# Kernel optimization log

Measured on AMD Instinct MI355X. Metric: run time of the kernel, lower is better.

Reference implementation:

```python
import jax, jax.numpy as jnp
import numpy as np

N_NODES = 50000      # also number of hyperedges (square incidence)
N_HEDGES = 50000
N_INC = 800000       # number of (node, hyperedge) incidences
N_LINKS = 20000
IN_DIM = 128         # edge_x dim; x dim is 2*IN_DIM
LATENT = [64, 64, 64]
HIDDEN = 256


def _hconv(x, src, dst, n_src, n_dst, W, b):
    """PyG HypergraphConv (no attention, unit hyperedge weights):
    out = D^{-1} H B^{-1} H^T (x W) + b, with src=node idx, dst=hyperedge idx."""
    xw = x @ W  # [n_src, out]
    ones = jnp.ones(src.shape[0], xw.dtype)
    Bdeg = jax.ops.segment_sum(ones, dst, num_segments=n_dst)
    Binv = jnp.where(Bdeg > 0, 1.0 / Bdeg, 0.0)
    Ddeg = jax.ops.segment_sum(ones, src, num_segments=n_src)
    Dinv = jnp.where(Ddeg > 0, 1.0 / Ddeg, 0.0)
    # node -> hyperedge aggregate, normalized by B^{-1}
    he = jax.ops.segment_sum(xw[src], dst, num_segments=n_dst) * Binv[:, None]
    # hyperedge -> node aggregate, normalized by D^{-1}
    out = jax.ops.segment_sum(he[dst], src, num_segments=n_src) * Dinv[:, None]
    return out + b


def setup_inputs() -> dict:
    key = jax.random.key(0)
    ks = jax.random.split(key, 24)
    inp = {
        "x": jax.random.normal(ks[0], (N_NODES, 2 * IN_DIM), jnp.float32),
        "edge_x": jax.random.normal(ks[1], (N_HEDGES, IN_DIM), jnp.float32),
        "edge_index": jax.random.randint(ks[2], (2, N_INC), 0, N_NODES, dtype=jnp.int32),
        "marks": jax.random.randint(ks[3], (N_LINKS,), 0, N_NODES, dtype=jnp.int32),
        "edge_marks": jax.random.randint(ks[4], (N_LINKS,), 0, N_HEDGES - 1, dtype=jnp.int32),
    }
    def lin(k, fin, fout):
        s = 1.0 / np.sqrt(fin)
        return jax.random.uniform(k, (fin, fout), jnp.float32, -s, s)
    # node convs: (2*IN_DIM -> 2*L0), (2*L0 -> 2*L1), (2*L1 -> 2*L2)
    nd = [2 * IN_DIM] + [2 * l for l in LATENT]
    ed = [IN_DIM] + list(LATENT)
    for i in range(3):
        inp[f"Wn{i}"] = lin(ks[5 + i], nd[i], nd[i + 1])
        inp[f"bn{i}"] = jnp.zeros((nd[i + 1],), jnp.float32)
        inp[f"We{i}"] = lin(ks[8 + i], ed[i], ed[i + 1])
        inp[f"be{i}"] = jnp.zeros((ed[i + 1],), jnp.float32)
    feat = sum(LATENT) * 4
    inp["W1"] = lin(ks[11], feat, HIDDEN)
    inp["b1"] = jnp.zeros((HIDDEN,), jnp.float32)
    inp["W2"] = lin(ks[12], HIDDEN, 2)
    inp["b2"] = jnp.zeros((2,), jnp.float32)
    return inp


def reference(x, edge_x, edge_index, marks, edge_marks,
              Wn0, bn0, Wn1, bn1, Wn2, bn2,
              We0, be0, We1, be1, We2, be2,
              W1, b1, W2, b2):
    nsrc, hdst = edge_index[0], edge_index[1]
    node_layers = [(Wn0, bn0), (Wn1, bn1), (Wn2, bn2)]
    edge_layers = [(We0, be0), (We1, be1), (We2, be2)]
    h, all_x = x, []
    for W, b in node_layers:
        h = jax.nn.relu(_hconv(h, nsrc, hdst, N_NODES, N_HEDGES, W, b))
        all_x.append(h)
    g, all_e = edge_x, []
    for W, b in edge_layers:  # flipped incidence: hyperedges act as nodes
        g = jax.nn.relu(_hconv(g, hdst, nsrc, N_HEDGES, N_NODES, W, b))
        all_e.append(g)
    xc = jnp.concatenate(all_x, axis=1)[marks]           # [L, 2*sum(latent)]
    ec = jnp.concatenate(all_e, axis=1)                  # [M, sum(latent)]
    a, b2_ = ec[edge_marks], ec[edge_marks + 1]
    feat = jnp.concatenate([jnp.minimum(a, b2_), jnp.maximum(a, b2_), xc], axis=1)
    h1 = jax.nn.relu(feat @ W1 + b1)
    logits = h1 @ W2 + b2
    return jax.nn.log_softmax(logits, axis=1)
```

## Files before the change

kernel.cpp:

```cpp
#include <hip/hip_runtime.h>
#include <hip/hip_fp16.h>
#include <math.h>

#define NN 50000
#define NH 50000
#define NI 800000
#define NL 20000

using half8 = __attribute__((ext_vector_type(8))) _Float16;
using f32x4 = __attribute__((ext_vector_type(4))) float;

static __device__ __forceinline__ float2 pack_h4(float4 v) {
    float2 st;
    *(__half2*)&st.x = __float22half2_rn(make_float2(v.x, v.y));
    *(__half2*)&st.y = __float22half2_rn(make_float2(v.z, v.w));
    return st;
}
static __device__ __forceinline__ void acc_h8(float4& a, float4& b, float4 raw) {
    const __half2* hp = (const __half2*)&raw;
    float2 f0 = __half22float2(hp[0]);
    float2 f1 = __half22float2(hp[1]);
    float2 f2 = __half22float2(hp[2]);
    float2 f3 = __half22float2(hp[3]);
    a.x += f0.x; a.y += f0.y; a.z += f1.x; a.w += f1.y;
    b.x += f2.x; b.y += f2.y; b.z += f3.x; b.w += f3.y;
}
static __device__ __forceinline__ float4 pack_h8(float4 a, float4 b) {
    float4 st;
    ((__half2*)&st)[0] = __float22half2_rn(make_float2(a.x, a.y));
    ((__half2*)&st)[1] = __float22half2_rn(make_float2(a.z, a.w));
    ((__half2*)&st)[2] = __float22half2_rn(make_float2(b.x, b.y));
    ((__half2*)&st)[3] = __float22half2_rn(make_float2(b.z, b.w));
    return st;
}

#define PB_X   12500
#define PB_EX  18750
#define PB_WT  19838
#define PB_H   22963
__global__ void k_prep(const float* __restrict__ x, __half* __restrict__ xh,
                       const float* __restrict__ ex, __half* __restrict__ exh,
                       const float* __restrict__ Wn0, const float* __restrict__ Wn1,
                       const float* __restrict__ Wn2, const float* __restrict__ We0,
                       const float* __restrict__ We1, const float* __restrict__ We2,
                       const float* __restrict__ W1,
                       __half* __restrict__ Wnt0, __half* __restrict__ Wnt1,
                       __half* __restrict__ Wnt2, __half* __restrict__ Wet0,
                       __half* __restrict__ Wet1, __half* __restrict__ Wet2,
                       __half* __restrict__ W1t,
                       const int* __restrict__ ei, int* __restrict__ cnt_n,
                       int* __restrict__ cnt_h) {
    int b = blockIdx.x, t = threadIdx.x;
    if (b < PB_X) {
        int i = b * 256 + t;
        float4 v = ((const float4*)x)[i];
        ((float2*)xh)[i] = pack_h4(v);
    } else if (b < PB_EX) {
        int i = (b - PB_X) * 256 + t;
        float4 v = ((const float4*)ex)[i];
        ((float2*)exh)[i] = pack_h4(v);
    } else if (b < PB_WT) {
        int u = (b - PB_EX) * 256 + t;
        if (u < 278528) {
            const float* S; __half* D; int K, N;
            if (u < 32768)      { S = Wn0; D = Wnt0; K = 256; N = 128; }
            else if (u < 49152) { S = Wn1; D = Wnt1; K = 128; N = 128; u -= 32768; }
            else if (u < 65536) { S = Wn2; D = Wnt2; K = 128; N = 128; u -= 49152; }
            else if (u < 73728) { S = We0; D = Wet0; K = 128; N = 64;  u -= 65536; }
            else if (u < 77824) { S = We1; D = Wet1; K = 64;  N = 64;  u -= 73728; }
            else if (u < 81920) { S = We2; D = Wet2; K = 64;  N = 64;  u -= 77824; }
            else                { S = W1;  D = W1t;  K = 768; N = 256; u -= 81920; }
            int n = u / K, k = u % K;
            D[(size_t)n * K + k] = __float2half(S[(size_t)k * N + n]);
        }
    } else {
        int e = (b - PB_WT) * 256 + t;
        if (e < NI) {
            atomicAdd(&cnt_n[ei[e]], 1);
            atomicAdd(&cnt_h[ei[e + NI]], 1);
        }
    }
}

__global__ void k_scanp1(const int* __restrict__ cnt_n, const int* __restrict__ cnt_h,
                         int* __restrict__ parts) {
    __shared__ int s[256];
    int arr = blockIdx.x / 196, blk = blockIdx.x % 196, t = threadIdx.x;
    const int* cnt = arr ? cnt_h : cnt_n;
    int i = blk * 256 + t;
    int v = (i < 50000) ? cnt[i] : 0;
    s[t] = v;
    __syncthreads();
#pragma unroll
    for (int d = 128; d > 0; d >>= 1) {
        if (t < d) s[t] += s[t + d];
        __syncthreads();
    }
    if (t == 0) parts[arr * 256 + blk] = s[0];
}

__global__ void k_scanp2(int* __restrict__ parts, int* __restrict__ off_n,
                         int* __restrict__ off_h) {
    __shared__ int s[256];
    int b = blockIdx.x, t = threadIdx.x;
    int* P = parts + b * 256;
    int v = (t < 196) ? P[t] : 0;
    s[t] = v;
    __syncthreads();
#pragma unroll
    for (int d = 1; d < 256; d <<= 1) {
        int u = (t >= d) ? s[t - d] : 0;
        __syncthreads();
        s[t] += u;
        __syncthreads();
    }
    if (t < 196) P[t] = s[t] - v;
    if (t == 0) {
        int* off = b ? off_h : off_n;
        off[50000] = s[255];
    }
}

__global__ void k_scanp3(const int* __restrict__ cnt_n, const int* __restrict__ cnt_h,
                         const int* __restrict__ parts, int* __restrict__ off_n,
                         int* __restrict__ off_h, float* __restrict__ invn,
                         float* __restrict__ invh) {
    __shared__ int s[256];
    int arr = blockIdx.x / 196, blk = blockIdx.x % 196, t = threadIdx.x;
    const int* cnt = arr ? cnt_h : cnt_n;
    int* off = arr ? off_h : off_n;
    float* inv = arr ? invh : invn;
    int i = blk * 256 + t;
    int c = (i < 50000) ? cnt[i] : 0;
    s[t] = c;
    __syncthreads();
#pragma unroll
    for (int d = 1; d < 256; d <<= 1) {
        int u = (t >= d) ? s[t - d] : 0;
        __syncthreads();
        s[t] += u;
        __syncthreads();
    }
    if (i < 50000) {
        off[i] = parts[arr * 256 + blk] + s[t] - c;
        inv[i] = c > 0 ? 1.0f / (float)c : 0.0f;
    }
}

#define FILL_SEGS 98
#define FILL_PER  8164
__global__ void k_fill(const int* __restrict__ ei, const int* __restrict__ off_n,
                       const int* __restrict__ off_h, int* __restrict__ cur_n,
                       int* __restrict__ cur_h, int* __restrict__ adj_n,
                       int* __restrict__ adj_h) {
    int bucket = blockIdx.x & 7;
    int seg = blockIdx.x >> 3;
    int lo = seg * FILL_PER;
    int hi = min(lo + FILL_PER, NI);
    for (int e = lo + (int)threadIdx.x; e < hi; e += 256) {
        int s = ei[e], d = ei[e + NI];
        if (d / 6250 == bucket) {
            int p = atomicAdd(&cur_h[d], 1);
            adj_h[off_h[d] + p] = s;
        }
        if (s / 6250 == bucket) {
            int q = atomicAdd(&cur_n[s], 1);
            adj_n[off_n[s] + q] = d;
        }
    }
}

template <int BM, int BN, int FM, int FN>
static __device__ __forceinline__ void gemm_body(const __half* __restrict__ X,
                                                 const __half* __restrict__ Wt,
                                                 __half* __restrict__ Y, int M, int K,
                                                 int blk, __half* smem) {
    constexpr int LDK = 56;
    constexpr int WN = BN / 4;
    __half* Xs = smem;
    __half* Ws = smem + BM * LDK;
    int t = threadIdx.x;
    int wave = t >> 6, lane = t & 63;
    int g = lane >> 4, lr = lane & 15;
    int bm0 = blk * BM;
    f32x4 acc[FM][FN] = {};

    for (int k0 = 0; k0 < K; k0 += 32) {
        for (int u = t; u < BM * 4; u += 256) {
            int r = u >> 2, q = u & 3;
            int rg = bm0 + r; if (rg >= M) rg = M - 1;
            *(float4*)&Xs[r * LDK + q * 8] = *(const float4*)&X[(size_t)rg * K + k0 + q * 8];
        }
        for (int u = t; u < BN * 4; u += 256) {
            int r = u >> 2, q = u & 3;
            *(float4*)&Ws[r * LDK + q * 8] = *(const float4*)&Wt[(size_t)r * K + k0 + q * 8];
        }
        __syncthreads();
        half8 a[FM], b[FN];
#pragma unroll
        for (int fm = 0; fm < FM; fm++)
            a[fm] = *(const half8*)&Xs[(fm * 16 + lr) * LDK + g * 8];
#pragma unroll
        for (int fn = 0; fn < FN; fn++)
            b[fn] = *(const half8*)&Ws[(wave * WN + fn * 16 + lr) * LDK + g * 8];
#pragma unroll
        for (int fm = 0; fm < FM; fm++)
#pragma unroll
            for (int fn = 0; fn < FN; fn++)
                acc[fm][fn] = __builtin_amdgcn_mfma_f32_16x16x32_f16(a[fm], b[fn], acc[fm][fn], 0, 0, 0);
        __syncthreads();
    }
#pragma unroll
    for (int fm = 0; fm < FM; fm++) {
#pragma unroll
        for (int fn = 0; fn < FN; fn++) {
            int cg = wave * WN + fn * 16 + lr;
#pragma unroll
            for (int reg = 0; reg < 4; reg++) {
                int rg = bm0 + fm * 16 + g * 4 + reg;
                if (rg < M) Y[(size_t)rg * BN + cg] = __float2half(acc[fm][fn][reg]);
            }
        }
    }
}

__global__ void __launch_bounds__(256)
k_gemm2(const __half* __restrict__ Xn, const __half* __restrict__ Wtn,
        __half* __restrict__ Yn, int Kn,
        const __half* __restrict__ Xe, const __half* __restrict__ Wte,
        __half* __restrict__ Ye, int Ke) {
    __shared__ __align__(16) __half smem[(64 + 128) * 56];
    if (blockIdx.x < 782)
        gemm_body<64, 128, 4, 2>(Xn, Wtn, Yn, NN, Kn, blockIdx.x, smem);
    else
        gemm_body<64, 64, 4, 1>(Xe, Wte, Ye, NH, Ke, blockIdx.x - 782, smem);
}

template <int F, bool RELU>
static __device__ __forceinline__ void pull_body(const __half* __restrict__ in,
                                                 const int* __restrict__ off,
                                                 const int* __restrict__ adj,
                                                 const float* __restrict__ scale,
                                                 const float* __restrict__ bias,
                                                 __half* __restrict__ out,
                                                 int nrows, int blk) {
    constexpr int TPR = F / 8;
    constexpr int RPB = 256 / TPR;
    int r = blk * RPB + (int)threadIdx.x / TPR;
    int lane = threadIdx.x % TPR;
    if (r >= nrows) return;
    int lo = off[r], hi = off[r + 1];
    const float4* in4 = (const float4*)in;
    float4 a0 = {0,0,0,0}, b0 = {0,0,0,0}, a1 = {0,0,0,0}, b1v = {0,0,0,0};
    float4 a2 = {0,0,0,0}, b2v = {0,0,0,0}, a3 = {0,0,0,0}, b3 = {0,0,0,0};
    int j = lo;
    for (; j + 7 < hi; j += 8) {
        int c0 = adj[j], c1 = adj[j + 1], c2 = adj[j + 2], c3 = adj[j + 3];
        int c4 = adj[j + 4], c5 = adj[j + 5], c6 = adj[j + 6], c7 = adj[j + 7];
        float4 v0 = in4[(size_t)c0 * TPR + lane];
        float4 v1 = in4[(size_t)c1 * TPR + lane];
        float4 v2 = in4[(size_t)c2 * TPR + lane];
        float4 v3 = in4[(size_t)c3 * TPR + lane];
        float4 v4 = in4[(size_t)c4 * TPR + lane];
        float4 v5 = in4[(size_t)c5 * TPR + lane];
        float4 v6 = in4[(size_t)c6 * TPR + lane];
        float4 v7 = in4[(size_t)c7 * TPR + lane];
        acc_h8(a0, b0, v0); acc_h8(a1, b1v, v1); acc_h8(a2, b2v, v2); acc_h8(a3, b3, v3);
        acc_h8(a0, b0, v4); acc_h8(a1, b1v, v5); acc_h8(a2, b2v, v6); acc_h8(a3, b3, v7);
    }
    for (; j + 1 < hi; j += 2) {
        int c0 = adj[j], c1 = adj[j + 1];
        float4 v0 = in4[(size_t)c0 * TPR + lane];
        float4 v1 = in4[(size_t)c1 * TPR + lane];
        acc_h8(a0, b0, v0); acc_h8(a1, b1v, v1);
    }
    if (j < hi) {
        float4 v0 = in4[(size_t)adj[j] * TPR + lane];
        acc_h8(a0, b0, v0);
    }
    a0.x += a1.x + a2.x + a3.x; a0.y += a1.y + a2.y + a3.y;
    a0.z += a1.z + a2.z + a3.z; a0.w += a1.w + a2.w + a3.w;
    b0.x += b1v.x + b2v.x + b3.x; b0.y += b1v.y + b2v.y + b3.y;
    b0.z += b1v.z + b2v.z + b3.z; b0.w += b1v.w + b2v.w + b3.w;
    float sc = scale[r];
    if (RELU) {
        float4 ba = ((const float4*)bias)[lane * 2];
        float4 bb = ((const float4*)bias)[lane * 2 + 1];
        a0.x = fmaxf(fmaf(a0.x, sc, ba.x), 0.f);
        a0.y = fmaxf(fmaf(a0.y, sc, ba.y), 0.f);
        a0.z = fmaxf(fmaf(a0.z, sc, ba.z), 0.f);
        a0.w = fmaxf(fmaf(a0.w, sc, ba.w), 0.f);
        b0.x = fmaxf(fmaf(b0.x, sc, bb.x), 0.f);
        b0.y = fmaxf(fmaf(b0.y, sc, bb.y), 0.f);
        b0.z = fmaxf(fmaf(b0.z, sc, bb.z), 0.f);
        b0.w = fmaxf(fmaf(b0.w, sc, bb.w), 0.f);
    } else {
        a0.x *= sc; a0.y *= sc; a0.z *= sc; a0.w *= sc;
        b0.x *= sc; b0.y *= sc; b0.z *= sc; b0.w *= sc;
    }
    ((float4*)out)[(size_t)r * TPR + lane] = pack_h8(a0, b0);
}

template <bool RELU>
__global__ void k_pull2(const __half* __restrict__ inA, const int* __restrict__ offA,
                        const int* __restrict__ adjA, const float* __restrict__ scA,
                        const float* __restrict__ biA, __half* __restrict__ outA, int rowsA,
                        const __half* __restrict__ inB, const int* __restrict__ offB,
                        const int* __restrict__ adjB, const float* __restrict__ scB,
                        const float* __restrict__ biB, __half* __restrict__ outB, int rowsB) {
    if (blockIdx.x < 3125)
        pull_body<128, RELU>(inA, offA, adjA, scA, biA, outA, rowsA, blockIdx.x);
    else
        pull_body<64, RELU>(inB, offB, adjB, scB, biB, outB, rowsB, blockIdx.x - 3125);
}

__global__ void __launch_bounds__(256)
k_mlp_mfma(const __half* __restrict__ hx1, const __half* __restrict__ hx2,
           const __half* __restrict__ hx3, const __half* __restrict__ gx1,
           const __half* __restrict__ gx2, const __half* __restrict__ gx3,
           const int* __restrict__ marks, const int* __restrict__ emarks,
           const __half* __restrict__ W1t, const float* __restrict__ b1,
           const float* __restrict__ W2, const float* __restrict__ b2,
           float* __restrict__ out) {
    constexpr int LDK = 56;
    __shared__ __align__(16) __half Xs[32 * LDK];
    __shared__ __align__(16) __half Ws[256 * LDK];
    __shared__ float part[4][32][2];
    int t = threadIdx.x;
    int wave = t >> 6, lane = t & 63;
    int g = lane >> 4, lr = lane & 15;
    int bm0 = blockIdx.x * 32;
    int r_s = t >> 2, q_s = t & 3;
    int m_s = 0, e_s = 0;
    if (t < 128) {
        int l = bm0 + r_s; if (l >= NL) l = NL - 1;
        m_s = marks[l]; e_s = emarks[l];
    }
    f32x4 acc[2][4] = {};

    for (int k0 = 0; k0 < 768; k0 += 32) {
        if (t < 128) {
            if (k0 < 384) {
                int fb = (k0 < 192 ? k0 : k0 - 192) + q_s * 8;
                const __half* gs = fb < 64 ? gx1 : (fb < 128 ? gx2 : gx3);
                int off = fb & 63;
                half8 va = *(const half8*)&gs[(size_t)e_s * 64 + off];
                half8 vb = *(const half8*)&gs[(size_t)(e_s + 1) * 64 + off];
                half8 rv;
                if (k0 < 192) {
#pragma unroll
                    for (int j = 0; j < 8; j++)
                        rv[j] = (_Float16)fminf((float)va[j], (float)vb[j]);
                } else {
#pragma unroll
                    for (int j = 0; j < 8; j++)
                        rv[j] = (_Float16)fmaxf((float)va[j], (float)vb[j]);
                }
                *(half8*)&Xs[r_s * LDK + q_s * 8] = rv;
            } else {
                int fb = (k0 - 384) + q_s * 8;
                const __half* hs = fb < 128 ? hx1 : (fb < 256 ? hx2 : hx3);
                int off = fb & 127;
                *(float4*)&Xs[r_s * LDK + q_s * 8] = *(const float4*)&hs[(size_t)m_s * 128 + off];
            }
        }
        for (int u = t; u < 1024; u += 256) {
            int r = u >> 2, q = u & 3;
            *(float4*)&Ws[r * LDK + q * 8] = *(const float4*)&W1t[(size_t)r * 768 + k0 + q * 8];
        }
        __syncthreads();
        half8 a[2], b[4];
#pragma unroll
        for (int fm = 0; fm < 2; fm++)
            a[fm] = *(const half8*)&Xs[(fm * 16 + lr) * LDK + g * 8];
#pragma unroll
        for (int fn = 0; fn < 4; fn++)
            b[fn] = *(const half8*)&Ws[(wave * 64 + fn * 16 + lr) * LDK + g * 8];
#pragma unroll
        for (int fm = 0; fm < 2; fm++)
#pragma unroll
            for (int fn = 0; fn < 4; fn++)
                acc[fm][fn] = __builtin_amdgcn_mfma_f32_16x16x32_f16(a[fm], b[fn], acc[fm][fn], 0, 0, 0);
        __syncthreads();
    }
    float b1c[4], w20[4], w21[4];
#pragma unroll
    for (int fn = 0; fn < 4; fn++) {
        int col = wave * 64 + fn * 16 + lr;
        b1c[fn] = b1[col];
        w20[fn] = W2[(size_t)col * 2 + 0];
        w21[fn] = W2[(size_t)col * 2 + 1];
    }
    float p0[2][4], p1[2][4];
#pragma unroll
    for (int fm = 0; fm < 2; fm++) {
#pragma unroll
        for (int reg = 0; reg < 4; reg++) {
            float s0 = 0.f, s1 = 0.f;
#pragma unroll
            for (int fn = 0; fn < 4; fn++) {
                float hh = fmaxf(acc[fm][fn][reg] + b1c[fn], 0.f);
                s0 = fmaf(hh, w20[fn], s0);
                s1 = fmaf(hh, w21[fn], s1);
            }
            p0[fm][reg] = s0; p1[fm][reg] = s1;
        }
    }
#pragma unroll
    for (int mask = 1; mask < 16; mask <<= 1) {
#pragma unroll
        for (int fm = 0; fm < 2; fm++)
#pragma unroll
            for (int reg = 0; reg < 4; reg++) {
                p0[fm][reg] += __shfl_xor(p0[fm][reg], mask);
                p1[fm][reg] += __shfl_xor(p1[fm][reg], mask);
            }
    }
    if (lr == 0) {
#pragma unroll
        for (int fm = 0; fm < 2; fm++)
#pragma unroll
            for (int reg = 0; reg < 4; reg++) {
                int row = fm * 16 + g * 4 + reg;
                part[wave][row][0] = p0[fm][reg];
                part[wave][row][1] = p1[fm][reg];
            }
    }
    __syncthreads();
    if (t < 32) {
        int l = bm0 + t;
        if (l < NL) {
            float l0 = part[0][t][0] + part[1][t][0] + part[2][t][0] + part[3][t][0] + b2[0];
            float l1 = part[0][t][1] + part[1][t][1] + part[2][t][1] + part[3][t][1] + b2[1];
            float mx = fmaxf(l0, l1);
            float lse = mx + logf(expf(l0 - mx) + expf(l1 - mx));
            out[(size_t)l * 2 + 0] = l0 - lse;
            out[(size_t)l * 2 + 1] = l1 - lse;
        }
    }
}

extern "C" void kernel_launch(void* const* d_in, const int* in_sizes, int n_in,
                              void* d_out, int out_size, void* d_ws, size_t ws_size,
                              hipStream_t stream) {
    const float* x      = (const float*)d_in[0];
    const float* ex     = (const float*)d_in[1];
    const int*   ei     = (const int*)d_in[2];
    const int*   marks  = (const int*)d_in[3];
    const int*   emarks = (const int*)d_in[4];
    const float* Wn[3] = {(const float*)d_in[5],  (const float*)d_in[9],  (const float*)d_in[13]};
    const float* bn[3] = {(const float*)d_in[6],  (const float*)d_in[10], (const float*)d_in[14]};
    const float* We[3] = {(const float*)d_in[7],  (const float*)d_in[11], (const float*)d_in[15]};
    const float* be[3] = {(const float*)d_in[8],  (const float*)d_in[12], (const float*)d_in[16]};
    const float* W1 = (const float*)d_in[17];
    const float* b1 = (const float*)d_in[18];
    const float* W2 = (const float*)d_in[19];
    const float* b2 = (const float*)d_in[20];

    int*    off_n = (int*)d_ws;
    int*    off_h = off_n + 50004;
    int*    adj_n = off_h + 50004;
    int*    adj_h = adj_n + 800000;
    int*    cnt   = adj_h + 800000;
    int*    cur   = cnt + 100000;
    int*    parts = cur + 100000;
    float*  invn  = (float*)(parts + 512);
    float*  invh  = invn + 50000;
    __half* xh    = (__half*)(invh + 50000);
    __half* exh   = xh + 12800000;
    __half* xwb   = exh + 6400000;
    __half* xwb2  = xwb + 6400000;
    __half* heb   = xwb2 + 3200000;
    __half* heb2  = heb + 6400000;
    __half* h[3]  = {heb2 + 3200000, heb2 + 9600000, heb2 + 16000000};
    __half* g[3]  = {h[2] + 6400000, h[2] + 9600000, h[2] + 12800000};
    __half* Wnt[3] = {g[2] + 3200000, g[2] + 3232768, g[2] + 3249152};
    __half* Wet[3] = {g[2] + 3265536, g[2] + 3273728, g[2] + 3277824};
    __half* W1t    = g[2] + 3281920;

    int* cnt_n = cnt;
    int* cnt_h = cnt + 50000;
    int* cur_n = cur;
    int* cur_h = cur + 50000;

    hipMemsetAsync(cnt, 0, 200000 * sizeof(int), stream);
    k_prep<<<PB_H, 256, 0, stream>>>(x, xh, ex, exh,
                                     Wn[0], Wn[1], Wn[2], We[0], We[1], We[2], W1,
                                     Wnt[0], Wnt[1], Wnt[2], Wet[0], Wet[1], Wet[2], W1t,
                                     ei, cnt_n, cnt_h);
    k_scanp1<<<392, 256, 0, stream>>>(cnt_n, cnt_h, parts);
    k_scanp2<<<2, 256, 0, stream>>>(parts, off_n, off_h);
    k_scanp3<<<392, 256, 0, stream>>>(cnt_n, cnt_h, parts, off_n, off_h, invn, invh);
    k_fill<<<FILL_SEGS * 8, 256, 0, stream>>>(ei, off_n, off_h, cur_n, cur_h, adj_n, adj_h);

    const __half* cn = xh;  int kn = 256;
    const __half* ce = exh; int ke = 128;
    for (int i = 0; i < 3; i++) {
        k_gemm2<<<1564, 256, 0, stream>>>(cn, Wnt[i], xwb, kn, ce, Wet[i], xwb2, ke);
        k_pull2<false><<<4688, 256, 0, stream>>>(xwb, off_h, adj_h, invh, nullptr, heb, NH,
                                                 xwb2, off_n, adj_n, invn, nullptr, heb2, NN);
        k_pull2<true><<<4688, 256, 0, stream>>>(heb, off_n, adj_n, invn, bn[i], h[i], NN,
                                                heb2, off_h, adj_h, invh, be[i], g[i], NH);
        cn = h[i]; kn = 128;
        ce = g[i]; ke = 64;
    }

    k_mlp_mfma<<<(NL + 31) / 32, 256, 0, stream>>>(h[0], h[1], h[2], g[0], g[1], g[2],
                                                   marks, emarks, W1t, b1, W2, b2, (float*)d_out);
}
```

Before: 582.9 us.

## Fuse fp32-to-fp16 input conversion into first GEMM and bucket degree histogram

The standalone conversion of x and edge_x to fp16 in the prep kernel is removed. The first-layer GEMM now loads fp32 tiles directly and packs them to half while filling shared memory, so the fp16 copies are never written to and re-read from global memory. The degree histogram is also restructured into segment-by-bucket blocks, so each block handles only atomics whose index falls in its bucket. This improves atomic locality, but every block now re-reads the edge indices across the eight buckets.

```diff
diff --git a/kernel.cpp b/kernel.cpp
--- a/kernel.cpp
+++ b/kernel.cpp
@@ -34,13 +34,10 @@
     return st;
 }
 
-#define PB_X   12500
-#define PB_EX  18750
-#define PB_WT  19838
-#define PB_H   22963
-__global__ void k_prep(const float* __restrict__ x, __half* __restrict__ xh,
-                       const float* __restrict__ ex, __half* __restrict__ exh,
-                       const float* __restrict__ Wn0, const float* __restrict__ Wn1,
+#define WT_BLKS 1088
+#define HIST_SEGS 98
+#define HIST_PER  8164
+__global__ void k_prep(const float* __restrict__ Wn0, const float* __restrict__ Wn1,
                        const float* __restrict__ Wn2, const float* __restrict__ We0,
                        const float* __restrict__ We1, const float* __restrict__ We2,
                        const float* __restrict__ W1,
@@ -51,16 +48,8 @@
                        const int* __restrict__ ei, int* __restrict__ cnt_n,
                        int* __restrict__ cnt_h) {
     int b = blockIdx.x, t = threadIdx.x;
-    if (b < PB_X) {
-        int i = b * 256 + t;
-        float4 v = ((const float4*)x)[i];
-        ((float2*)xh)[i] = pack_h4(v);
-    } else if (b < PB_EX) {
-        int i = (b - PB_X) * 256 + t;
-        float4 v = ((const float4*)ex)[i];
-        ((float2*)exh)[i] = pack_h4(v);
-    } else if (b < PB_WT) {
-        int u = (b - PB_EX) * 256 + t;
+    if (b < WT_BLKS) {
+        int u = b * 256 + t;
         if (u < 278528) {
             const float* S; __half* D; int K, N;
             if (u < 32768)      { S = Wn0; D = Wnt0; K = 256; N = 128; }
@@ -74,10 +63,15 @@
             D[(size_t)n * K + k] = __float2half(S[(size_t)k * N + n]);
         }
     } else {
-        int e = (b - PB_WT) * 256 + t;
-        if (e < NI) {
-            atomicAdd(&cnt_n[ei[e]], 1);
-            atomicAdd(&cnt_h[ei[e + NI]], 1);
+        int hb = b - WT_BLKS;
+        int bucket = hb & 7;
+        int seg = hb >> 3;
+        int lo = seg * HIST_PER;
+        int hi = min(lo + HIST_PER, NI);
+        for (int e = lo + t; e < hi; e += 256) {
+            int s = ei[e], d = ei[e + NI];
+            if (s / 6250 == bucket) atomicAdd(&cnt_n[s], 1);
+            if (d / 6250 == bucket) atomicAdd(&cnt_h[d], 1);
         }
     }
 }
@@ -170,8 +164,8 @@
     }
 }
 
-template <int BM, int BN, int FM, int FN>
-static __device__ __forceinline__ void gemm_body(const __half* __restrict__ X,
+template <typename SrcT, int BM, int BN, int FM, int FN>
+static __device__ __forceinline__ void gemm_body(const SrcT* __restrict__ X,
                                                  const __half* __restrict__ Wt,
                                                  __half* __restrict__ Y, int M, int K,
                                                  int blk, __half* smem) {
@@ -189,7 +183,16 @@
         for (int u = t; u < BM * 4; u += 256) {
             int r = u >> 2, q = u & 3;
             int rg = bm0 + r; if (rg >= M) rg = M - 1;
-            *(float4*)&Xs[r * LDK + q * 8] = *(const float4*)&X[(size_t)rg * K + k0 + q * 8];
+            if constexpr (sizeof(SrcT) == 4) {
+                const float* src = (const float*)X + (size_t)rg * K + k0 + q * 8;
+                float4 v0 = *(const float4*)src;
+                float4 v1 = *(const float4*)(src + 4);
+                *(float2*)&Xs[r * LDK + q * 8]     = pack_h4(v0);
+                *(float2*)&Xs[r * LDK + q * 8 + 4] = pack_h4(v1);
+            } else {
+                *(float4*)&Xs[r * LDK + q * 8] =
+                    *(const float4*)((const __half*)X + (size_t)rg * K + k0 + q * 8);
+            }
         }
         for (int u = t; u < BN * 4; u += 256) {
             int r = u >> 2, q = u & 3;
@@ -224,16 +227,17 @@
     }
 }
 
+template <typename SrcT>
 __global__ void __launch_bounds__(256)
-k_gemm2(const __half* __restrict__ Xn, const __half* __restrict__ Wtn,
+k_gemm2(const SrcT* __restrict__ Xn, const __half* __restrict__ Wtn,
         __half* __restrict__ Yn, int Kn,
-        const __half* __restrict__ Xe, const __half* __restrict__ Wte,
+        const SrcT* __restrict__ Xe, const __half* __restrict__ Wte,
         __half* __restrict__ Ye, int Ke) {
     __shared__ __align__(16) __half smem[(64 + 128) * 56];
     if (blockIdx.x < 782)
-        gemm_body<64, 128, 4, 2>(Xn, Wtn, Yn, NN, Kn, blockIdx.x, smem);
+        gemm_body<SrcT, 64, 128, 4, 2>(Xn, Wtn, Yn, NN, Kn, blockIdx.x, smem);
     else
-        gemm_body<64, 64, 4, 1>(Xe, Wte, Ye, NH, Ke, blockIdx.x - 782, smem);
+        gemm_body<SrcT, 64, 64, 4, 1>(Xe, Wte, Ye, NH, Ke, blockIdx.x - 782, smem);
 }
 
 template <int F, bool RELU>
@@ -466,9 +470,7 @@
     int*    parts = cur + 100000;
     float*  invn  = (float*)(parts + 512);
     float*  invh  = invn + 50000;
-    __half* xh    = (__half*)(invh + 50000);
-    __half* exh   = xh + 12800000;
-    __half* xwb   = exh + 6400000;
+    __half* xwb   = (__half*)(invh + 50000);
     __half* xwb2  = xwb + 6400000;
     __half* heb   = xwb2 + 3200000;
     __half* heb2  = heb + 6400000;
@@ -484,25 +486,27 @@
     int* cur_h = cur + 50000;
 
     hipMemsetAsync(cnt, 0, 200000 * sizeof(int), stream);
-    k_prep<<<PB_H, 256, 0, stream>>>(x, xh, ex, exh,
-                                     Wn[0], Wn[1], Wn[2], We[0], We[1], We[2], W1,
-                                     Wnt[0], Wnt[1], Wnt[2], Wet[0], Wet[1], Wet[2], W1t,
-                                     ei, cnt_n, cnt_h);
+    k_prep<<<WT_BLKS + HIST_SEGS * 8, 256, 0, stream>>>(
+        Wn[0], Wn[1], Wn[2], We[0], We[1], We[2], W1,
+        Wnt[0], Wnt[1], Wnt[2], Wet[0], Wet[1], Wet[2], W1t,
+        ei, cnt_n, cnt_h);
     k_scanp1<<<392, 256, 0, stream>>>(cnt_n, cnt_h, parts);
     k_scanp2<<<2, 256, 0, stream>>>(parts, off_n, off_h);
     k_scanp3<<<392, 256, 0, stream>>>(cnt_n, cnt_h, parts, off_n, off_h, invn, invh);
     k_fill<<<FILL_SEGS * 8, 256, 0, stream>>>(ei, off_n, off_h, cur_n, cur_h, adj_n, adj_h);
 
-    const __half* cn = xh;  int kn = 256;
-    const __half* ce = exh; int ke = 128;
-    for (int i = 0; i < 3; i++) {
-        k_gemm2<<<1564, 256, 0, stream>>>(cn, Wnt[i], xwb, kn, ce, Wet[i], xwb2, ke);
+    k_gemm2<float><<<1564, 256, 0, stream>>>(x, Wnt[0], xwb, 256, ex, Wet[0], xwb2, 128);
+    k_pull2<false><<<4688, 256, 0, stream>>>(xwb, off_h, adj_h, invh, nullptr, heb, NH,
+                                             xwb2, off_n, adj_n, invn, nullptr, heb2, NN);
+    k_pull2<true><<<4688, 256, 0, stream>>>(heb, off_n, adj_n, invn, bn[0], h[0], NN,
+                                            heb2, off_h, adj_h, invh, be[0], g[0], NH);
+    for (int i = 1; i < 3; i++) {
+        k_gemm2<__half><<<1564, 256, 0, stream>>>(h[i - 1], Wnt[i], xwb, 128,
+                                                  g[i - 1], Wet[i], xwb2, 64);
         k_pull2<false><<<4688, 256, 0, stream>>>(xwb, off_h, adj_h, invh, nullptr, heb, NH,
                                                  xwb2, off_n, adj_n, invn, nullptr, heb2, NN);
         k_pull2<true><<<4688, 256, 0, stream>>>(heb, off_n, adj_n, invn, bn[i], h[i], NN,
                                                 heb2, off_h, adj_h, invh, be[i], g[i], NH);
-        cn = h[i]; kn = 128;
-        ce = g[i]; ke = 64;
     }
 
     k_mlp_mfma<<<(NL + 31) / 32, 256, 0, stream>>>(h[0], h[1], h[2], g[0], g[1], g[2],
```

Result: faster. 571.3 us (-2.0%).
